# Kernel optimization log

Measured on AMD Instinct MI355X. Metric: run time of the kernel, lower is better.

Reference implementation:

```python
import jax, jax.numpy as jnp
import numpy as np

KERNEL_MUL = 2.0
KERNEL_NUM = 5
EPS = 1e-3


def setup_inputs() -> dict:
    key = jax.random.key(0)
    k1, k2 = jax.random.split(key)
    source = jax.random.normal(k1, (2048, 512), dtype=jnp.float32)
    target = jax.random.normal(k2, (2048, 512), dtype=jnp.float32)
    beta = jnp.ones((KERNEL_NUM,), dtype=jnp.float32) / KERNEL_NUM
    return {"source": source, "target": target, "beta": beta}


def _sq_dists(total):
    # squared Euclidean pairwise distances, (N, N), clamped >= 0 (matches cdist(p=2)**2)
    sq = jnp.sum(total * total, axis=-1)
    d = sq[:, None] + sq[None, :] - 2.0 * (total @ total.T)
    return jnp.maximum(d, 0.0)


def _project_simplex(v):
    m = v.shape[0]
    mu = -jnp.sort(-v)                      # descending
    cs = jnp.cumsum(mu)
    ar = jnp.arange(1, m + 1, dtype=v.dtype)
    cond = mu - (cs - 1.0) / ar > 0
    idx = jnp.where(cond, jnp.arange(m), -1)
    rho = jnp.where(jnp.any(cond), jnp.max(idx), 0)
    theta = (cs[rho] - 1.0) / (rho + 1).astype(v.dtype)
    p = jnp.maximum(v - theta, 0.0)
    return p / (p.sum() + 1e-12)


def _update_beta(source, target, beta):
    # Batched version of the per-pair quad-kernel loop in _update_beta.
    Ns, D = source.shape
    Nt = target.shape[0]
    P = min(Ns // 2, Nt // 2)  # num_effective_pairs (static)
    s = source[: 2 * P].reshape(P, 2, D)
    t = target[: 2 * P].reshape(P, 2, D)
    quad = jnp.concatenate([s, t], axis=1)              # (P, 4, D) -> [s1, s2, t1, t2]
    diff = quad[:, :, None, :] - quad[:, None, :, :]
    sq = jnp.sum(diff * diff, axis=-1)                  # (P, 4, 4)
    offdiag = ~np.eye(4, dtype=bool)
    bw = jnp.median(sq[:, offdiag], axis=1) + 1e-6      # per-pair median of nonzero dists
    bw = bw / (KERNEL_MUL ** (KERNEL_NUM // 2))
    bws = bw[:, None] * (KERNEL_MUL ** jnp.arange(KERNEL_NUM, dtype=bw.dtype))[None, :]
    K = jnp.exp(-sq[:, None, :, :] / bws[:, :, None, None])   # (P, 5, 4, 4)
    g = K[:, :, 0, 1] + K[:, :, 2, 3] - K[:, :, 0, 2] - K[:, :, 1, 3]  # (P, 5)
    gm = jnp.mean(g, axis=0)
    Q = (g.T @ g) / P - jnp.outer(gm, gm) + EPS * jnp.eye(KERNEL_NUM, dtype=g.dtype)
    # projected gradient descent on the simplex (lr=1, max_iter=100, tol=1e-6)
    def cond_fn(st):
        _, _, i, conv = st
        return (i < 100) & (~conv)
    def body_fn(st):
        b, _, i, _ = st
        proj = _project_simplex(b - Q @ b)
        conv = jnp.linalg.norm(proj - b) < 1e-6
        return (proj, proj, i + 1, conv)
    _, proj, _, _ = jax.lax.while_loop(
        cond_fn, body_fn, (beta, beta, jnp.int32(0), jnp.array(False)))
    return proj


def _forward(source, target, beta):
    beta_new = _update_beta(jax.lax.stop_gradient(source),
                            jax.lax.stop_gradient(target), beta)
    Ns = source.shape[0]
    total = jnp.concatenate([source, target], axis=0)   # (N, D)
    N = total.shape[0]
    sq = _sq_dists(total)                               # (N, N)
    offdiag = ~np.eye(N, dtype=bool)
    bw = jnp.median(sq[offdiag]) + 1e-6
    bw = bw / (KERNEL_MUL ** (KERNEL_NUM // 2))
    bws = bw * (KERNEL_MUL ** jnp.arange(KERNEL_NUM, dtype=sq.dtype))  # (5,)
    Ks = jnp.exp(-sq[None, :, :] / bws[:, None, None])  # (5, N, N)
    joint = jnp.einsum('k,kij->ij', beta_new, Ks)
    XX = joint[:Ns, :Ns]
    YY = joint[Ns:, Ns:]
    XY = joint[:Ns, Ns:]
    n = XX.shape[0]
    m = YY.shape[0]
    term_XX = (jnp.sum(XX) - jnp.trace(XX)) / (n * (n - 1))
    term_YY = (jnp.sum(YY) - jnp.trace(YY)) / (m * (m - 1))
    term_XY = jnp.sum(XY) / (n * m)
    loss = term_XX + term_YY - 2.0 * term_XY
    return jnp.maximum(loss, 0.0)


def reference(source, target, beta):
    return _forward(source, target, beta)
```

## Files before the change

### kernel.cpp

```cpp
#include <hip/hip_runtime.h>
#include <math.h>

#define NT 4096
#define NS 2048
#define DDIM 512
#define KN 5
#define NTILES 528

typedef __bf16 bf16x8 __attribute__((ext_vector_type(8)));
typedef float f32x4 __attribute__((ext_vector_type(4)));
typedef unsigned short u16x8 __attribute__((ext_vector_type(8)));

static __device__ inline unsigned short f2bf(float x) {
    unsigned u = __float_as_uint(x);
    unsigned r = (u + 0x7fffu + ((u >> 16) & 1u)) >> 16;
    return (unsigned short)r;
}
static __device__ inline float bf2f(unsigned short h) {
    return __uint_as_float(((unsigned)h) << 16);
}

static __device__ inline void tri_map(int b, int& bx, int& by) {
    int x = (int)((sqrtf(8.0f * (float)b + 1.0f) - 1.0f) * 0.5f);
    while ((x + 1) * (x + 2) / 2 <= b) ++x;
// ... 61 lines not shown
#define CMPSW(x, y) { float hi_ = fmaxf(x, y); float lo_ = fminf(x, y); x = hi_; y = lo_; }
        CMPSW(mu0, mu1) CMPSW(mu3, mu4) CMPSW(mu2, mu4) CMPSW(mu2, mu3)
        CMPSW(mu0, mu3) CMPSW(mu0, mu2) CMPSW(mu1, mu4) CMPSW(mu1, mu3) CMPSW(mu1, mu2)
#undef CMPSW
        float cs0 = mu0, cs1 = cs0 + mu1, cs2 = cs1 + mu2, cs3 = cs2 + mu3, cs4 = cs3 + mu4;
        bool c1 = mu1 * 2.0f > cs1 - 1.0f;
        bool c2 = mu2 * 3.0f > cs2 - 1.0f;
        bool c3 = mu3 * 4.0f > cs3 - 1.0f;
        bool c4 = mu4 * 5.0f > cs4 - 1.0f;
        float csSel = cs0, rcpSel = 1.0f;
        if (c1) { csSel = cs1; rcpSel = 0.5f; }
        if (c2) { csSel = cs2; rcpSel = (1.0f / 3.0f); }
        if (c3) { csSel = cs3; rcpSel = 0.25f; }
        if (c4) { csSel = cs4; rcpSel = 0.2f; }
        float theta = (csSel - 1.0f) * rcpSel;
        float ssum = 0.0f;
        #pragma unroll
        for (int k = 0; k < KN; ++k) { proj[k] = fmaxf(v[k] - theta, 0.0f); ssum += proj[k]; }
        float invs = 1.0f / (ssum + 1e-12f);
        float nd = 0.0f;
        #pragma unroll
        for (int k = 0; k < KN; ++k) {
            proj[k] *= invs;
            float dd = proj[k] - b[k];
            nd += dd * dd;
            b[k] = proj[k];
        }
        if (nd < 1e-12f) break;
    }
    #pragma unroll
    for (int k = 0; k < KN; ++k) beta_out[k] = proj[k];
}

__global__ __launch_bounds__(256) void k_prep2(const float* __restrict__ S,
                                               const float* __restrict__ T,
                                               unsigned short* __restrict__ Hi,
                                               unsigned short* __restrict__ Lo,
                                               float* __restrict__ norms,
                                               float* __restrict__ g,
                                               unsigned* __restrict__ hists,
                                               unsigned* __restrict__ sel)
{
    if (blockIdx.x < 44) hists[blockIdx.x * 256 + threadIdx.x] = 0;
    if (blockIdx.x == 50 && threadIdx.x == 0) {
        sel[0] = 0u; sel[1] = 8386559u;
        sel[2] = 0u; sel[3] = 8386560u;
    }
    int p = blockIdx.x * 4 + (threadIdx.x >> 6);
    int l = threadIdx.x & 63;
    const float* r0 = S + (size_t)(2 * p) * DDIM;
    const float* r1 = r0 + DDIM;
    const float* r2 = T + (size_t)(2 * p) * DDIM;
    const float* r3 = r2 + DDIM;
    float a[8], b[8], c[8], d[8];
    *(float4*)&a[0] = *(const float4*)(r0 + l * 8); *(float4*)&a[4] = *(const float4*)(r0 + l * 8 + 4);
    *(float4*)&b[0] = *(const float4*)(r1 + l * 8); *(float4*)&b[4] = *(const float4*)(r1 + l * 8 + 4);
    *(float4*)&c[0] = *(const float4*)(r2 + l * 8); *(float4*)&c[4] = *(const float4*)(r2 + l * 8 + 4);
    *(float4*)&d[0] = *(const float4*)(r3 + l * 8); *(float4*)&d[4] = *(const float4*)(r3 + l * 8 + 4);

    float n0 = 0, n1 = 0, n2 = 0, n3 = 0;
    float s01 = 0, s23 = 0, s02 = 0, s13 = 0, s03 = 0, s12 = 0;
    u16x8 h0, l0, h1, l1, h2, l2, h3, l3;
    #pragma unroll
    for (int k = 0; k < 8; ++k) {
        float va = a[k], vb = b[k], vc = c[k], vd = d[k];
        n0 += va * va; n1 += vb * vb; n2 += vc * vc; n3 += vd * vd;
        float t01 = va - vb, t23 = vc - vd, t02 = va - vc, t13 = vb - vd;
        s01 += t01*t01; s23 += t23*t23; s02 += t02*t02; s13 += t13*t13;
        float t03 = va - vd, t12 = vb - vc;
        s03 += t03*t03; s12 += t12*t12;
        unsigned short hh;
        hh = f2bf(va); h0[k] = hh; l0[k] = f2bf(va - bf2f(hh));
        hh = f2bf(vb); h1[k] = hh; l1[k] = f2bf(vb - bf2f(hh));
        hh = f2bf(vc); h2[k] = hh; l2[k] = f2bf(vc - bf2f(hh));
        hh = f2bf(vd); h3[k] = hh; l3[k] = f2bf(vd - bf2f(hh));
    }
// ... 5 lines not shown
    *(u16x8*)&Hi[g1] = h1; *(u16x8*)&Lo[g1] = l1;
    *(u16x8*)&Hi[g2] = h2; *(u16x8*)&Lo[g2] = l2;
    *(u16x8*)&Hi[g3] = h3; *(u16x8*)&Lo[g3] = l3;

    #pragma unroll
    for (int m = 32; m > 0; m >>= 1) {
        n0 += __shfl_xor(n0, m); n1 += __shfl_xor(n1, m);
        n2 += __shfl_xor(n2, m); n3 += __shfl_xor(n3, m);
        s01 += __shfl_xor(s01, m); s23 += __shfl_xor(s23, m);
        s02 += __shfl_xor(s02, m); s13 += __shfl_xor(s13, m);
        s03 += __shfl_xor(s03, m); s12 += __shfl_xor(s12, m);
    }
    if (l == 0) {
        norms[2 * p] = n0; norms[2 * p + 1] = n1;
        norms[NS + 2 * p] = n2; norms[NS + 2 * p + 1] = n3;
        float v[6] = { s01, s02, s03, s12, s13, s23 };
        for (int i = 0; i < 5; ++i)
            for (int j = 0; j < 5 - i; ++j)
                if (v[j] > v[j + 1]) { float t = v[j]; v[j] = v[j + 1]; v[j + 1] = t; }
        float med = 0.5f * (v[2] + v[3]);
        float bw = (med + 1e-6f) * 0.25f;
        #pragma unroll
        for (int k = 0; k < KN; ++k) {
            float inv = 1.0f / (bw * (float)(1 << k));
            g[(size_t)p * KN + k] = expf(-s01 * inv) + expf(-s23 * inv)
                                  - expf(-s02 * inv) - expf(-s13 * inv);
        }
    }
}

__global__ __launch_bounds__(256) void k_dist_mfma(const unsigned short* __restrict__ Hi,
                                                   const unsigned short* __restrict__ Lo,
                                                   const float* __restrict__ norms,
                                                   float* __restrict__ D,
                                                   const float* __restrict__ g,
                                                   const float* __restrict__ beta_in,
                                                   float* __restrict__ beta_out)
{
    __shared__ __align__(16) unsigned short sA[2][2][128][32];
    __shared__ __align__(16) unsigned short sB[2][2][128][32];

    if (blockIdx.x == 0) {
        if (threadIdx.x < 64) beta_solve(g, beta_in, beta_out);
        return;
    }

    int bb = blockIdx.x - 1;
    int swz = (bb & 7) * 66 + (bb >> 3);
    int bx, by;
    tri_map(swz, bx, by);
    const int m0 = by * 128, n0 = bx * 128;

    const int tid = threadIdx.x;
    const int w = tid >> 6, l = tid & 63;
    const int wr = w >> 1, wc = w & 1;

    const int chunk = (l & 3) ^ ((((l >> 2) & 3) + ((l >> 4) & 3)) & 3);
    const size_t gA0 = (size_t)(m0 + w * 16 + (l >> 2)) * DDIM + chunk * 8;
    const size_t gA1 = gA0 + (size_t)64 * DDIM;
    const size_t gB0 = (size_t)(n0 + w * 16 + (l >> 2)) * DDIM + chunk * 8;
    const size_t gB1 = gB0 + (size_t)64 * DDIM;
    const unsigned w1024 = w * 1024;

#define GLD(dst, srcptr, goff)                                                      \
    __builtin_amdgcn_global_load_lds(                                               \
        (const __attribute__((address_space(1))) unsigned*)((srcptr) + (goff)),     \
        (__attribute__((address_space(3))) unsigned*)((char*)(dst) + w1024), 16, 0, 0)
#define STAGE(buf, kk)                                  \
    do {                                                \
        GLD(&sA[buf][0][0][0],  Hi, gA0 + (kk));        \
        GLD(&sA[buf][0][64][0], Hi, gA1 + (kk));        \
        GLD(&sA[buf][1][0][0],  Lo, gA0 + (kk));        \
        GLD(&sA[buf][1][64][0], Lo, gA1 + (kk));        \
        GLD(&sB[buf][0][0][0],  Hi, gB0 + (kk));        \
        GLD(&sB[buf][0][64][0], Hi, gB1 + (kk));        \
        GLD(&sB[buf][1][0][0],  Lo, gB0 + (kk));        \
        GLD(&sB[buf][1][64][0], Lo, gB1 + (kk));        \
    } while (0)

    f32x4 acc[4][4] = {};
    const int q = l >> 4;
    const int fr = ((l & 3) + ((l >> 2) & 3)) & 3;
    const unsigned soff = ((unsigned)(q ^ fr)) << 4;
    const unsigned rowbA = (wr * 64 + (l & 15)) * 64 + soff;
    const unsigned rowbB = (wc * 64 + (l & 15)) * 64 + soff;

    STAGE(0, 0);
    __syncthreads();

    #pragma unroll 2
    for (int t = 0; t < 16; ++t) {
        const int cur = t & 1;
        if (t < 15) STAGE(cur ^ 1, (t + 1) * 32);

        bf16x8 ah[4], al[4], bh[4], bl[4];
        #pragma unroll
        for (int m = 0; m < 4; ++m) {
            ah[m] = *(const bf16x8*)((const char*)&sA[cur][0][0][0] + rowbA + m * 1024);
            al[m] = *(const bf16x8*)((const char*)&sA[cur][1][0][0] + rowbA + m * 1024);
        }
        #pragma unroll
        for (int n = 0; n < 4; ++n) {
            bh[n] = *(const bf16x8*)((const char*)&sB[cur][0][0][0] + rowbB + n * 1024);
            bl[n] = *(const bf16x8*)((const char*)&sB[cur][1][0][0] + rowbB + n * 1024);
        }
        #pragma unroll
        for (int m = 0; m < 4; ++m)
            #pragma unroll
            for (int n = 0; n < 4; ++n) {
                acc[m][n] = __builtin_amdgcn_mfma_f32_16x16x32_bf16(bh[n], ah[m], acc[m][n], 0, 0, 0);
                acc[m][n] = __builtin_amdgcn_mfma_f32_16x16x32_bf16(bl[n], ah[m], acc[m][n], 0, 0, 0);
                acc[m][n] = __builtin_amdgcn_mfma_f32_16x16x32_bf16(bh[n], al[m], acc[m][n], 0, 0, 0);
            }
        __syncthreads();
    }
#undef STAGE
#undef GLD

    float* rowbuf = (float*)&sA[0][0][0][0] + w * 1024;
    const int rr = l & 15;
    #pragma unroll
    for (int m = 0; m < 4; ++m) {
        float nrm = norms[m0 + wr * 64 + m * 16 + rr];
        #pragma unroll
        for (int n = 0; n < 4; ++n) {
            int cb = n0 + wc * 64 + n * 16 + (q << 2);
            float4 ncv = *(const float4*)&norms[cb];
            f32x4 a = acc[m][n];
            float4 o;
            o.x = fmaxf(nrm + ncv.x - 2.0f * a[0], 0.0f);
            o.y = fmaxf(nrm + ncv.y - 2.0f * a[1], 0.0f);
            o.z = fmaxf(nrm + ncv.z - 2.0f * a[2], 0.0f);
            o.w = fmaxf(nrm + ncv.w - 2.0f * a[3], 0.0f);
            int ch = (n * 4 + q) ^ (rr & 7);
            *(float4*)(rowbuf + rr * 64 + ch * 4) = o;
        }
        #pragma unroll
        for (int s = 0; s < 4; ++s) {
            int row = s * 4 + q;
            int ch = (l & 15) ^ (row & 7);
            float4 v = *(const float4*)(rowbuf + row * 64 + ch * 4);
            *(float4*)&D[(size_t)(m0 + wr * 64 + m * 16 + row) * NT + n0 + wc * 64 + (l & 15) * 4] = v;
        }
    }
}

__global__ __launch_bounds__(256) void k_hist0_tri(const float* __restrict__ D,
                                                   unsigned* __restrict__ gH)
{
    __shared__ unsigned h[1024];
    for (int i = threadIdx.x; i < 1024; i += 256) h[i] = 0;
    int bx, by;
    tri_map(blockIdx.x, bx, by);
    int m0 = by * 128, n0 = bx * 128;
    unsigned wt = (bx != by) ? 2u : 1u;
    __syncthreads();
    for (int v = threadIdx.x; v < 4096; v += 256) {
        int r = m0 + (v >> 5);
        int c0 = n0 + (v & 31) * 4;
        float4 dv = *(const float4*)&D[(size_t)r * NT + c0];
        const float* dd = (const float*)&dv;
        unsigned pb = __float_as_uint(dd[0]) >> 22;
        unsigned pc = (r == c0) ? 0u : wt;
        #pragma unroll
        for (int j = 1; j < 4; ++j) {
            unsigned bj = __float_as_uint(dd[j]) >> 22;
            unsigned cj = (r == c0 + j) ? 0u : wt;
            if (bj == pb) pc += cj;
            else {
                if (pc) atomicAdd(&h[pb], pc);
                pb = bj; pc = cj;
            }
        }
        if (pc) atomicAdd(&h[pb], pc);
    }
    __syncthreads();
    for (int i = threadIdx.x; i < 1024; i += 256) {
        unsigned c = h[i];
        if (c) atomicAdd(&gH[i], c);
    }
}

__global__ __launch_bounds__(64) void k_scan0(const unsigned* __restrict__ hL0,
                                              unsigned* __restrict__ sel)
{
    int lane = threadIdx.x;
    for (int t = 0; t < 2; ++t) {
        unsigned r = sel[t * 2 + 1];
        unsigned s = 0;
        for (int i = 0; i < 16; ++i) s += hL0[lane * 16 + i];
        unsigned x = s;
        #pragma unroll
        for (int off = 1; off < 64; off <<= 1) {
            unsigned y = __shfl_up(x, off);
            if (lane >= off) x += y;
        }
        unsigned base = x - s;
        bool has = (r >= base) && (r < base + s);
        unsigned long long mm = __ballot(has);
        int leader = __ffsll(mm) - 1;
        unsigned bin = 0, cb = 0;
        if (lane == leader) {
            unsigned cc = base;
            for (int i = 0; i < 16; ++i) {
                unsigned hv = hL0[lane * 16 + i];
                if (r < cc + hv) { bin = lane * 16 + i; cb = cc; break; }
                cc += hv;
            }
        }
        bin = __shfl(bin, leader);
        cb = __shfl(cb, leader);
        if (lane == 0) {
            sel[t * 2 + 0] = bin;
            sel[t * 2 + 1] = r - cb;
        }
    }
}

template<int LEVEL>
__global__ __launch_bounds__(256) void k_hist_tri(const float* __restrict__ D,
                                                  const unsigned* __restrict__ sel,
                                                  unsigned* __restrict__ gA,
                                                  unsigned* __restrict__ gB)
{
    constexpr int NB = (LEVEL == 2) ? 4096 : 1024;
    __shared__ unsigned lha[NB];
    __shared__ unsigned lhb[NB];
    for (int i = threadIdx.x; i < NB; i += 256) { lha[i] = 0; lhb[i] = 0; }
    unsigned pA = sel[0], pB = sel[2];
    int bx, by;
    tri_map(blockIdx.x, bx, by);
    int m0 = by * 128, n0 = bx * 128;
    unsigned wt = (bx != by) ? 2u : 1u;
    __syncthreads();
    for (int v = threadIdx.x; v < 4096; v += 256) {
        int r = m0 + (v >> 5);
        int c0 = n0 + (v & 31) * 4;
        float4 dv = *(const float4*)&D[(size_t)r * NT + c0];
        const float* dd = (const float*)&dv;
        #pragma unroll
        for (int j = 0; j < 4; ++j) {
            if (r == c0 + j) continue;
            unsigned key = __float_as_uint(dd[j]);
            if constexpr (LEVEL == 1) {
                if ((key >> 22) == pA) atomicAdd(&lha[(key >> 12) & 1023], wt);
                if ((key >> 22) == pB) atomicAdd(&lhb[(key >> 12) & 1023], wt);
            } else {
                if ((key >> 12) == pA) atomicAdd(&lha[key & 4095], wt);
                if ((key >> 12) == pB) atomicAdd(&lhb[key & 4095], wt);
            }
        }
    }
    __syncthreads();
    for (int i = threadIdx.x; i < NB; i += 256) {
        unsigned ca = lha[i];
        if (ca) atomicAdd(&gA[i], ca);
        unsigned cb = lhb[i];
        if (cb) atomicAdd(&gB[i], cb);
    }
}

template<int LEVEL>
__global__ __launch_bounds__(64) void k_scan(const unsigned* __restrict__ hA,
                                             const unsigned* __restrict__ hB,
                                             unsigned* __restrict__ sel,
                                             float* __restrict__ params)
{
    constexpr int NB = (LEVEL == 2) ? 4096 : 1024;
    constexpr int C = NB / 64;
    int lane = threadIdx.x;
    for (int t = 0; t < 2; ++t) {
        const unsigned* h = (t == 0 ? hA : hB);
        unsigned r = sel[t * 2 + 1];
        unsigned s = 0;
        for (int i = 0; i < C; ++i) s += h[lane * C + i];
        unsigned x = s;
        #pragma unroll
        for (int off = 1; off < 64; off <<= 1) {
            unsigned y = __shfl_up(x, off);
            if (lane >= off) x += y;
        }
        unsigned base = x - s;
        bool has = (r >= base) && (r < base + s);
        unsigned long long mm = __ballot(has);
        int leader = __ffsll(mm) - 1;
        unsigned bin = 0, cb = 0;
        if (lane == leader) {
            unsigned cc = base;
            for (int i = 0; i < C; ++i) {
                unsigned hv = h[lane * C + i];
                if (r < cc + hv) { bin = lane * C + i; cb = cc; break; }
                cc += hv;
            }
        }
        bin = __shfl(bin, leader);
        cb = __shfl(cb, leader);
        if (lane == 0) {
            if (LEVEL == 1) sel[t * 2 + 0] = (sel[t * 2 + 0] << 10) | bin;
            else            sel[4 + t]     = (sel[t * 2 + 0] << 12) | bin;
            sel[t * 2 + 1] = r - cb;
        }
    }
    if (LEVEL == 2 && lane == 0) {
        float vA = __uint_as_float(sel[4]);
        float vB = __uint_as_float(sel[5]);
        float med = 0.5f * (vA + vB);
        float bw = (med + 1e-6f) * 0.25f;
        #pragma unroll
        for (int k = 0; k < KN; ++k) params[k] = 1.0f / (bw * (float)(1 << k));
    }
}

__global__ __launch_bounds__(256) void k_wsum_tri(const float* __restrict__ D,
                                                  const float* __restrict__ params,
                                                  const float* __restrict__ beta,
                                                  double* __restrict__ partials)
{
    float i0 = params[0], i1 = params[1], i2 = params[2], i3 = params[3], i4 = params[4];
    float b0 = beta[0], b1 = beta[1], b2 = beta[2], b3 = beta[3], b4 = beta[4];
    const double wDiag = 1.0 / ((double)NS * (NS - 1));
    const double wOff = -1.0 / ((double)NS * NS);
    int bx, by;
    tri_map(blockIdx.x, bx, by);
    int m0 = by * 128, n0 = bx * 128;
    double wt = (bx != by) ? 2.0 : 1.0;
    double acc = 0.0;
    for (int v = threadIdx.x; v < 4096; v += 256) {
        int r = m0 + (v >> 5);
        int c0 = n0 + (v & 31) * 4;
        float4 dv = *(const float4*)&D[(size_t)r * NT + c0];
        const float* dd = (const float*)&dv;
        #pragma unroll
        for (int j = 0; j < 4; ++j) {
            int c = c0 + j;
            if (r == c) continue;
            float sq = dd[j];
            float val = b0 * __expf(-sq * i0) + b1 * __expf(-sq * i1) + b2 * __expf(-sq * i2)
                      + b3 * __expf(-sq * i3) + b4 * __expf(-sq * i4);
            bool same = (r < NS) == (c < NS);
            acc += (same ? wDiag : wOff) * (double)val;
        }
    }
    acc *= wt;
    __shared__ double red[256];
    red[threadIdx.x] = acc;
    __syncthreads();
    for (int off = 128; off > 0; off >>= 1) {
        if (threadIdx.x < off) red[threadIdx.x] += red[threadIdx.x + off];
        __syncthreads();
    }
    if (threadIdx.x == 0) partials[blockIdx.x] = red[0];
}

__global__ __launch_bounds__(256) void k_final(const double* __restrict__ partials,
                                               float* __restrict__ out, int count)
{
    double acc = 0;
    for (int i = threadIdx.x; i < count; i += 256) acc += partials[i];
    __shared__ double red[256];
    red[threadIdx.x] = acc;
    __syncthreads();
    for (int off = 128; off > 0; off >>= 1) {
        if (threadIdx.x < off) red[threadIdx.x] += red[threadIdx.x + off];
        __syncthreads();
    }
    if (threadIdx.x == 0) out[0] = (float)fmax(red[0], 0.0);
}

extern "C" void kernel_launch(void* const* d_in, const int* in_sizes, int n_in,
                              void* d_out, int out_size, void* d_ws, size_t ws_size,
                              hipStream_t stream)
{
    const float* S = (const float*)d_in[0];
    const float* T = (const float*)d_in[1];
    const float* beta = (const float*)d_in[2];
    float* out = (float*)d_out;

    float* D = (float*)d_ws;
    unsigned short* Hi = (unsigned short*)(D + (size_t)NT * NT);
    unsigned short* Lo = Hi + (size_t)NT * DDIM;
    float* norms = (float*)(Lo + (size_t)NT * DDIM);
    float* g = norms + NT;
    float* beta2 = g + 1024 * KN;
    float* params = beta2 + 8;
    unsigned* sel = (unsigned*)(params + 8);
    unsigned* hists = sel + 16;
    unsigned* hL0 = hists;
    unsigned* hL1A = hL0 + 1024;
    unsigned* hL1B = hL1A + 1024;
    unsigned* hL2A = hL1B + 1024;
    unsigned* hL2B = hL2A + 4096;
    double* partials = (double*)(hists + 11264);

    k_prep2<<<dim3(256), dim3(256), 0, stream>>>(S, T, Hi, Lo, norms, g, hists, sel);
    k_dist_mfma<<<dim3(NTILES + 1), dim3(256), 0, stream>>>(Hi, Lo, norms, D, g, beta, beta2);
    k_hist0_tri<<<dim3(NTILES), dim3(256), 0, stream>>>(D, hL0);
    k_scan0<<<dim3(1), dim3(64), 0, stream>>>(hL0, sel);
    k_hist_tri<1><<<dim3(NTILES), dim3(256), 0, stream>>>(D, sel, hL1A, hL1B);
    k_scan<1><<<dim3(1), dim3(64), 0, stream>>>(hL1A, hL1B, sel, params);
    k_hist_tri<2><<<dim3(NTILES), dim3(256), 0, stream>>>(D, sel, hL2A, hL2B);
    k_scan<2><<<dim3(1), dim3(64), 0, stream>>>(hL2A, hL2B, sel, params);
    k_wsum_tri<<<dim3(NTILES), dim3(256), 0, stream>>>(D, params, beta2, partials);
    k_final<<<dim3(1), dim3(256), 0, stream>>>(partials, out, NTILES);
}
```

Baseline: 151.7 us.

## Fold scan kernels into histogram tails and triple-buffer GEMM staging

The separate single-block scan and final-reduce kernels are removed. The last block of each histogram or weighted-sum kernel, found with an atomic ticket counter, now does the scan or final reduction itself, which cuts ten launches to six. The distance GEMM moves from double to triple-buffered LDS staging with explicit vmcnt waits and a single barrier per k-step, and the beta solve moves into the first histogram kernel. This removes launch gaps and per-iteration sync stalls, at the cost of more LDS per block (lower occupancy) and reliance on threadfence/atomic ordering.

```diff
diff --git a/kernel.cpp b/kernel.cpp
--- a/kernel.cpp
+++ b/kernel.cpp
@@ -117,6 +117,35 @@
     for (int k = 0; k < KN; ++k) beta_out[k] = proj[k];
 }
 
+static __device__ void scan_find(unsigned* __restrict__ h, int C, unsigned r,
+                                 unsigned& bin, unsigned& rem)
+{
+    int lane = threadIdx.x;
+    unsigned s = 0;
+    for (int i = 0; i < C; ++i) s += atomicAdd(&h[lane * C + i], 0u);
+    unsigned x = s;
+    #pragma unroll
+    for (int off = 1; off < 64; off <<= 1) {
+        unsigned y = __shfl_up(x, off);
+        if (lane >= off) x += y;
+    }
+    unsigned base = x - s;
+    bool has = (r >= base) && (r < base + s);
+    unsigned long long mm = __ballot(has);
+    int leader = __ffsll(mm) - 1;
+    unsigned b = 0, cb = 0;
+    if (lane == leader) {
+        unsigned cc = base;
+        for (int i = 0; i < C; ++i) {
+            unsigned hv = atomicAdd(&h[lane * C + i], 0u);
+            if (r < cc + hv) { b = lane * C + i; cb = cc; break; }
+            cc += hv;
+        }
+    }
+    bin = __shfl(b, leader);
+    rem = r - __shfl(cb, leader);
+}
+
 __global__ __launch_bounds__(256) void k_prep2(const float* __restrict__ S,
                                                const float* __restrict__ T,
                                                unsigned short* __restrict__ Hi,
@@ -126,7 +155,7 @@
                                                unsigned* __restrict__ hists,
                                                unsigned* __restrict__ sel)
 {
-    if (blockIdx.x < 44) hists[blockIdx.x * 256 + threadIdx.x] = 0;
+    if (blockIdx.x < 45) hists[blockIdx.x * 256 + threadIdx.x] = 0;
     if (blockIdx.x == 50 && threadIdx.x == 0) {
         sel[0] = 0u; sel[1] = 8386559u;
         sel[2] = 0u; sel[3] = 8386560u;
@@ -198,20 +227,12 @@
 __global__ __launch_bounds__(256) void k_dist_mfma(const unsigned short* __restrict__ Hi,
                                                    const unsigned short* __restrict__ Lo,
                                                    const float* __restrict__ norms,
-                                                   float* __restrict__ D,
-                                                   const float* __restrict__ g,
-                                                   const float* __restrict__ beta_in,
-                                                   float* __restrict__ beta_out)
-{
-    __shared__ __align__(16) unsigned short sA[2][2][128][32];
-    __shared__ __align__(16) unsigned short sB[2][2][128][32];
-
-    if (blockIdx.x == 0) {
-        if (threadIdx.x < 64) beta_solve(g, beta_in, beta_out);
-        return;
-    }
-
-    int bb = blockIdx.x - 1;
+                                                   float* __restrict__ D)
+{
+    __shared__ __align__(16) unsigned short sA[3][2][128][32];
+    __shared__ __align__(16) unsigned short sB[3][2][128][32];
+
+    int bb = blockIdx.x;
     int swz = (bb & 7) * 66 + (bb >> 3);
     int bx, by;
     tri_map(swz, bx, by);
@@ -252,12 +273,16 @@
     const unsigned rowbB = (wc * 64 + (l & 15)) * 64 + soff;
 
     STAGE(0, 0);
-    __syncthreads();
-
-    #pragma unroll 2
+    STAGE(1, 32);
+
+    #pragma unroll 16
     for (int t = 0; t < 16; ++t) {
-        const int cur = t & 1;
-        if (t < 15) STAGE(cur ^ 1, (t + 1) * 32);
+        const int cur = t % 3;
+        if (t == 15) { asm volatile("s_waitcnt vmcnt(0)" ::: "memory"); }
+        else         { asm volatile("s_waitcnt vmcnt(8)" ::: "memory"); }
+        __builtin_amdgcn_s_barrier();
+        __builtin_amdgcn_sched_barrier(0);
+        if (t < 14) STAGE((t + 2) % 3, (t + 2) * 32);
 
         bf16x8 ah[4], al[4], bh[4], bl[4];
         #pragma unroll
@@ -278,10 +303,10 @@
                 acc[m][n] = __builtin_amdgcn_mfma_f32_16x16x32_bf16(bl[n], ah[m], acc[m][n], 0, 0, 0);
                 acc[m][n] = __builtin_amdgcn_mfma_f32_16x16x32_bf16(bh[n], al[m], acc[m][n], 0, 0, 0);
             }
-        __syncthreads();
     }
 #undef STAGE
 #undef GLD
+    __syncthreads();
 
     float* rowbuf = (float*)&sA[0][0][0][0] + w * 1024;
     const int rr = l & 15;
@@ -311,13 +336,23 @@
     }
 }
 
-__global__ __launch_bounds__(256) void k_hist0_tri(const float* __restrict__ D,
-                                                   unsigned* __restrict__ gH)
-{
+__global__ __launch_bounds__(256) void k_h0s(const float* __restrict__ D,
+                                             const float* __restrict__ g,
+                                             const float* __restrict__ beta_in,
+                                             float* __restrict__ beta_out,
+                                             unsigned* __restrict__ gH,
+                                             unsigned* __restrict__ sel,
+                                             unsigned* __restrict__ cnt)
+{
+    if (blockIdx.x == 0) {
+        if (threadIdx.x < 64) beta_solve(g, beta_in, beta_out);
+        return;
+    }
     __shared__ unsigned h[1024];
+    __shared__ unsigned tk;
     for (int i = threadIdx.x; i < 1024; i += 256) h[i] = 0;
     int bx, by;
-    tri_map(blockIdx.x, bx, by);
+    tri_map(blockIdx.x - 1, bx, by);
     int m0 = by * 128, n0 = bx * 128;
     unsigned wt = (bx != by) ? 2u : 1u;
     __syncthreads();
@@ -345,54 +380,31 @@
         unsigned c = h[i];
         if (c) atomicAdd(&gH[i], c);
     }
-}
-
-__global__ __launch_bounds__(64) void k_scan0(const unsigned* __restrict__ hL0,
-                                              unsigned* __restrict__ sel)
-{
-    int lane = threadIdx.x;
-    for (int t = 0; t < 2; ++t) {
-        unsigned r = sel[t * 2 + 1];
-        unsigned s = 0;
-        for (int i = 0; i < 16; ++i) s += hL0[lane * 16 + i];
-        unsigned x = s;
-        #pragma unroll
-        for (int off = 1; off < 64; off <<= 1) {
-            unsigned y = __shfl_up(x, off);
-            if (lane >= off) x += y;
-        }
-        unsigned base = x - s;
-        bool has = (r >= base) && (r < base + s);
-        unsigned long long mm = __ballot(has);
-        int leader = __ffsll(mm) - 1;
-        unsigned bin = 0, cb = 0;
-        if (lane == leader) {
-            unsigned cc = base;
-            for (int i = 0; i < 16; ++i) {
-                unsigned hv = hL0[lane * 16 + i];
-                if (r < cc + hv) { bin = lane * 16 + i; cb = cc; break; }
-                cc += hv;
+    __syncthreads();
+    if (threadIdx.x == 0) { __threadfence(); tk = atomicAdd(&cnt[0], 1u); }
+    __syncthreads();
+    if (tk == NTILES - 1) {
+        __threadfence();
+        if (threadIdx.x < 64) {
+            for (int t = 0; t < 2; ++t) {
+                unsigned bin, rem;
+                scan_find(gH, 16, sel[t * 2 + 1], bin, rem);
+                if (threadIdx.x == 0) { sel[t * 2 + 0] = bin; sel[t * 2 + 1] = rem; }
             }
         }
-        bin = __shfl(bin, leader);
-        cb = __shfl(cb, leader);
-        if (lane == 0) {
-            sel[t * 2 + 0] = bin;
-            sel[t * 2 + 1] = r - cb;
-        }
-    }
-}
-
-template<int LEVEL>
-__global__ __launch_bounds__(256) void k_hist_tri(const float* __restrict__ D,
-                                                  const unsigned* __restrict__ sel,
-                                                  unsigned* __restrict__ gA,
-                                                  unsigned* __restrict__ gB)
-{
-    constexpr int NB = (LEVEL == 2) ? 4096 : 1024;
-    __shared__ unsigned lha[NB];
-    __shared__ unsigned lhb[NB];
-    for (int i = threadIdx.x; i < NB; i += 256) { lha[i] = 0; lhb[i] = 0; }
+    }
+}
+
+__global__ __launch_bounds__(256) void k_h1s(const float* __restrict__ D,
+                                             unsigned* __restrict__ sel,
+                                             unsigned* __restrict__ gA,
+                                             unsigned* __restrict__ gB,
+                                             unsigned* __restrict__ cnt)
+{
+    __shared__ unsigned lha[1024];
+    __shared__ unsigned lhb[1024];
+    __shared__ unsigned tk;
+    for (int i = threadIdx.x; i < 1024; i += 256) { lha[i] = 0; lhb[i] = 0; }
     unsigned pA = sel[0], pB = sel[2];
     int bx, by;
     tri_map(blockIdx.x, bx, by);
@@ -408,80 +420,104 @@
         for (int j = 0; j < 4; ++j) {
             if (r == c0 + j) continue;
             unsigned key = __float_as_uint(dd[j]);
-            if constexpr (LEVEL == 1) {
-                if ((key >> 22) == pA) atomicAdd(&lha[(key >> 12) & 1023], wt);
-                if ((key >> 22) == pB) atomicAdd(&lhb[(key >> 12) & 1023], wt);
-            } else {
-                if ((key >> 12) == pA) atomicAdd(&lha[key & 4095], wt);
-                if ((key >> 12) == pB) atomicAdd(&lhb[key & 4095], wt);
-            }
-        }
-    }
-    __syncthreads();
-    for (int i = threadIdx.x; i < NB; i += 256) {
+            if ((key >> 22) == pA) atomicAdd(&lha[(key >> 12) & 1023], wt);
+            if ((key >> 22) == pB) atomicAdd(&lhb[(key >> 12) & 1023], wt);
+        }
+    }
+    __syncthreads();
+    for (int i = threadIdx.x; i < 1024; i += 256) {
         unsigned ca = lha[i];
         if (ca) atomicAdd(&gA[i], ca);
         unsigned cb = lhb[i];
         if (cb) atomicAdd(&gB[i], cb);
     }
-}
-
-template<int LEVEL>
-__global__ __launch_bounds__(64) void k_scan(const unsigned* __restrict__ hA,
-                                             const unsigned* __restrict__ hB,
+    __syncthreads();
+    if (threadIdx.x == 0) { __threadfence(); tk = atomicAdd(&cnt[1], 1u); }
+    __syncthreads();
+    if (tk == NTILES - 1) {
+        __threadfence();
+        if (threadIdx.x < 64) {
+            for (int t = 0; t < 2; ++t) {
+                unsigned bin, rem;
+                scan_find(t == 0 ? gA : gB, 16, sel[t * 2 + 1], bin, rem);
+                if (threadIdx.x == 0) {
+                    sel[t * 2 + 0] = (sel[t * 2 + 0] << 10) | bin;
+                    sel[t * 2 + 1] = rem;
+                }
+            }
+        }
+    }
+}
+
+__global__ __launch_bounds__(256) void k_h2s(const float* __restrict__ D,
                                              unsigned* __restrict__ sel,
-                                             float* __restrict__ params)
-{
-    constexpr int NB = (LEVEL == 2) ? 4096 : 1024;
-    constexpr int C = NB / 64;
-    int lane = threadIdx.x;
-    for (int t = 0; t < 2; ++t) {
-        const unsigned* h = (t == 0 ? hA : hB);
-        unsigned r = sel[t * 2 + 1];
-        unsigned s = 0;
-        for (int i = 0; i < C; ++i) s += h[lane * C + i];
-        unsigned x = s;
-        #pragma unroll
-        for (int off = 1; off < 64; off <<= 1) {
-            unsigned y = __shfl_up(x, off);
-            if (lane >= off) x += y;
-        }
-        unsigned base = x - s;
-        bool has = (r >= base) && (r < base + s);
-        unsigned long long mm = __ballot(has);
-        int leader = __ffsll(mm) - 1;
-        unsigned bin = 0, cb = 0;
-        if (lane == leader) {
-            unsigned cc = base;
-            for (int i = 0; i < C; ++i) {
-                unsigned hv = h[lane * C + i];
-                if (r < cc + hv) { bin = lane * C + i; cb = cc; break; }
-                cc += hv;
+                                             unsigned* __restrict__ gA,
+                                             unsigned* __restrict__ gB,
+                                             float* __restrict__ params,
+                                             unsigned* __restrict__ cnt)
+{
+    __shared__ unsigned lha[4096];
+    __shared__ unsigned lhb[4096];
+    __shared__ unsigned tk;
+    for (int i = threadIdx.x; i < 4096; i += 256) { lha[i] = 0; lhb[i] = 0; }
+    unsigned pA = sel[0], pB = sel[2];
+    int bx, by;
+    tri_map(blockIdx.x, bx, by);
+    int m0 = by * 128, n0 = bx * 128;
+    unsigned wt = (bx != by) ? 2u : 1u;
+    __syncthreads();
+    for (int v = threadIdx.x; v < 4096; v += 256) {
+        int r = m0 + (v >> 5);
+        int c0 = n0 + (v & 31) * 4;
+        float4 dv = *(const float4*)&D[(size_t)r * NT + c0];
+        const float* dd = (const float*)&dv;
+        #pragma unroll
+        for (int j = 0; j < 4; ++j) {
+            if (r == c0 + j) continue;
+            unsigned key = __float_as_uint(dd[j]);
+            if ((key >> 12) == pA) atomicAdd(&lha[key & 4095], wt);
+            if ((key >> 12) == pB) atomicAdd(&lhb[key & 4095], wt);
+        }
+    }
+    __syncthreads();
+    for (int i = threadIdx.x; i < 4096; i += 256) {
+        unsigned ca = lha[i];
+        if (ca) atomicAdd(&gA[i], ca);
+        unsigned cb = lhb[i];
+        if (cb) atomicAdd(&gB[i], cb);
+    }
+    __syncthreads();
+    if (threadIdx.x == 0) { __threadfence(); tk = atomicAdd(&cnt[2], 1u); }
+    __syncthreads();
+    if (tk == NTILES - 1) {
+        __threadfence();
+        if (threadIdx.x < 64) {
+            unsigned keyA = 0, keyB = 0;
+            for (int t = 0; t < 2; ++t) {
+                unsigned bin, rem;
+                scan_find(t == 0 ? gA : gB, 64, sel[t * 2 + 1], bin, rem);
+                unsigned key = (sel[t * 2 + 0] << 12) | bin;
+                if (t == 0) keyA = key; else keyB = key;
             }
-        }
-        bin = __shfl(bin, leader);
-        cb = __shfl(cb, leader);
-        if (lane == 0) {
-            if (LEVEL == 1) sel[t * 2 + 0] = (sel[t * 2 + 0] << 10) | bin;
-            else            sel[4 + t]     = (sel[t * 2 + 0] << 12) | bin;
-            sel[t * 2 + 1] = r - cb;
-        }
-    }
-    if (LEVEL == 2 && lane == 0) {
-        float vA = __uint_as_float(sel[4]);
-        float vB = __uint_as_float(sel[5]);
-        float med = 0.5f * (vA + vB);
-        float bw = (med + 1e-6f) * 0.25f;
-        #pragma unroll
-        for (int k = 0; k < KN; ++k) params[k] = 1.0f / (bw * (float)(1 << k));
-    }
-}
-
-__global__ __launch_bounds__(256) void k_wsum_tri(const float* __restrict__ D,
-                                                  const float* __restrict__ params,
-                                                  const float* __restrict__ beta,
-                                                  double* __restrict__ partials)
-{
+            if (threadIdx.x == 0) {
+                float med = 0.5f * (__uint_as_float(keyA) + __uint_as_float(keyB));
+                float bw = (med + 1e-6f) * 0.25f;
+                #pragma unroll
+                for (int k = 0; k < KN; ++k) params[k] = 1.0f / (bw * (float)(1 << k));
+            }
+        }
+    }
+}
+
+__global__ __launch_bounds__(256) void k_wsumf(const float* __restrict__ D,
+                                               const float* __restrict__ params,
+                                               const float* __restrict__ beta,
+                                               double* __restrict__ partials,
+                                               unsigned* __restrict__ cnt,
+                                               float* __restrict__ out)
+{
+    __shared__ double red[256];
+    __shared__ unsigned tk;
     float i0 = params[0], i1 = params[1], i2 = params[2], i3 = params[3], i4 = params[4];
     float b0 = beta[0], b1 = beta[1], b2 = beta[2], b3 = beta[3], b4 = beta[4];
     const double wDiag = 1.0 / ((double)NS * (NS - 1));
@@ -508,29 +544,33 @@
         }
     }
     acc *= wt;
-    __shared__ double red[256];
     red[threadIdx.x] = acc;
     __syncthreads();
     for (int off = 128; off > 0; off >>= 1) {
         if (threadIdx.x < off) red[threadIdx.x] += red[threadIdx.x + off];
         __syncthreads();
     }
-    if (threadIdx.x == 0) partials[blockIdx.x] = red[0];
-}
-
-__global__ __launch_bounds__(256) void k_final(const double* __restrict__ partials,
-                                               float* __restrict__ out, int count)
-{
-    double acc = 0;
-    for (int i = threadIdx.x; i < count; i += 256) acc += partials[i];
-    __shared__ double red[256];
-    red[threadIdx.x] = acc;
-    __syncthreads();
-    for (int off = 128; off > 0; off >>= 1) {
-        if (threadIdx.x < off) red[threadIdx.x] += red[threadIdx.x + off];
+    if (threadIdx.x == 0) {
+        partials[blockIdx.x] = red[0];
+        __threadfence();
+        tk = atomicAdd(&cnt[3], 1u);
+    }
+    __syncthreads();
+    if (tk == NTILES - 1) {
+        __threadfence();
+        double a2 = 0.0;
+        for (int i = threadIdx.x; i < NTILES; i += 256) {
+            unsigned long long u = atomicAdd((unsigned long long*)&partials[i], 0ull);
+            a2 += __longlong_as_double(u);
+        }
+        red[threadIdx.x] = a2;
         __syncthreads();
-    }
-    if (threadIdx.x == 0) out[0] = (float)fmax(red[0], 0.0);
+        for (int off = 128; off > 0; off >>= 1) {
+            if (threadIdx.x < off) red[threadIdx.x] += red[threadIdx.x + off];
+            __syncthreads();
+        }
+        if (threadIdx.x == 0) out[0] = (float)fmax(red[0], 0.0);
+    }
 }
 
 extern "C" void kernel_launch(void* const* d_in, const int* in_sizes, int n_in,
@@ -552,20 +592,17 @@
     unsigned* sel = (unsigned*)(params + 8);
     unsigned* hists = sel + 16;
     unsigned* hL0 = hists;
-    unsigned* hL1A = hL0 + 1024;
-    unsigned* hL1B = hL1A + 1024;
-    unsigned* hL2A = hL1B + 1024;
-    unsigned* hL2B = hL2A + 4096;
-    double* partials = (double*)(hists + 11264);
+    unsigned* hL1A = hists + 1024;
+    unsigned* hL1B = hists + 2048;
+    unsigned* hL2A = hists + 3072;
+    unsigned* hL2B = hists + 7168;
+    unsigned* cnt  = hists + 11264;
+    double* partials = (double*)(hists + 11520);
 
     k_prep2<<<dim3(256), dim3(256), 0, stream>>>(S, T, Hi, Lo, norms, g, hists, sel);
-    k_dist_mfma<<<dim3(NTILES + 1), dim3(256), 0, stream>>>(Hi, Lo, norms, D, g, beta, beta2);
-    k_hist0_tri<<<dim3(NTILES), dim3(256), 0, stream>>>(D, hL0);
-    k_scan0<<<dim3(1), dim3(64), 0, stream>>>(hL0, sel);
-    k_hist_tri<1><<<dim3(NTILES), dim3(256), 0, stream>>>(D, sel, hL1A, hL1B);
-    k_scan<1><<<dim3(1), dim3(64), 0, stream>>>(hL1A, hL1B, sel, params);
-    k_hist_tri<2><<<dim3(NTILES), dim3(256), 0, stream>>>(D, sel, hL2A, hL2B);
-    k_scan<2><<<dim3(1), dim3(64), 0, stream>>>(hL2A, hL2B, sel, params);
-    k_wsum_tri<<<dim3(NTILES), dim3(256), 0, stream>>>(D, params, beta2, partials);
-    k_final<<<dim3(1), dim3(256), 0, stream>>>(partials, out, NTILES);
-}
+    k_dist_mfma<<<dim3(NTILES), dim3(256), 0, stream>>>(Hi, Lo, norms, D);
+    k_h0s<<<dim3(NTILES + 1), dim3(256), 0, stream>>>(D, g, beta, beta2, hL0, sel, cnt);
+    k_h1s<<<dim3(NTILES), dim3(256), 0, stream>>>(D, sel, hL1A, hL1B, cnt);
+    k_h2s<<<dim3(NTILES), dim3(256), 0, stream>>>(D, sel, hL2A, hL2B, params, cnt);
+    k_wsumf<<<dim3(NTILES), dim3(256), 0, stream>>>(D, params, beta2, partials, cnt, out);
+}
```

Result: slower. 202.7 us (+33.7%).

## Restructure median radix select with bf16 key copy and 12/4/16-bit levels

Applied to the files above, without the earlier changes.

The distance kernel now also writes a truncated 16-bit copy of each distance when the workspace is large enough. The first two histogram passes read this half-width copy instead of the fp32 matrix. The radix split changes from 10/10/12 to 12/4/16 bits, with a 65536-bin global-atomic histogram in the last pass and a 256-thread scan kernel. Norms are cached in shared memory in the distance epilogue. This cuts DRAM reads in two of the three selection passes, at the cost of an extra 32MB write, more zeroing work and global atomics in the final pass.

```diff
diff --git a/kernel.cpp b/kernel.cpp
--- a/kernel.cpp
+++ b/kernel.cpp
@@ -117,6 +117,7 @@
     for (int k = 0; k < KN; ++k) beta_out[k] = proj[k];
 }
 
+#define NZERO (4096 + 64 + 64 + 65536 + 65536)
 __global__ __launch_bounds__(256) void k_prep2(const float* __restrict__ S,
                                                const float* __restrict__ T,
                                                unsigned short* __restrict__ Hi,
@@ -126,7 +127,7 @@
                                                unsigned* __restrict__ hists,
                                                unsigned* __restrict__ sel)
 {
-    if (blockIdx.x < 44) hists[blockIdx.x * 256 + threadIdx.x] = 0;
+    for (unsigned i = blockIdx.x * 256 + threadIdx.x; i < NZERO; i += 65536) hists[i] = 0;
     if (blockIdx.x == 50 && threadIdx.x == 0) {
         sel[0] = 0u; sel[1] = 8386559u;
         sel[2] = 0u; sel[3] = 8386560u;
@@ -199,6 +200,8 @@
                                                    const unsigned short* __restrict__ Lo,
                                                    const float* __restrict__ norms,
                                                    float* __restrict__ D,
+                                                   unsigned short* __restrict__ D16,
+                                                   int do16,
                                                    const float* __restrict__ g,
                                                    const float* __restrict__ beta_in,
                                                    float* __restrict__ beta_out)
@@ -283,15 +286,19 @@
 #undef STAGE
 #undef GLD
 
+    float* ncache = (float*)&sB[0][0][0][0];
+    if (tid < 128) ncache[tid] = norms[m0 + tid];
+    else           ncache[tid] = norms[n0 + tid - 128];
+    __syncthreads();
+
     float* rowbuf = (float*)&sA[0][0][0][0] + w * 1024;
     const int rr = l & 15;
     #pragma unroll
     for (int m = 0; m < 4; ++m) {
-        float nrm = norms[m0 + wr * 64 + m * 16 + rr];
+        float nrm = ncache[wr * 64 + m * 16 + rr];
         #pragma unroll
         for (int n = 0; n < 4; ++n) {
-            int cb = n0 + wc * 64 + n * 16 + (q << 2);
-            float4 ncv = *(const float4*)&norms[cb];
+            float4 ncv = *(const float4*)&ncache[128 + wc * 64 + n * 16 + (q << 2)];
             f32x4 a = acc[m][n];
             float4 o;
             o.x = fmaxf(nrm + ncv.x - 2.0f * a[0], 0.0f);
@@ -306,171 +313,259 @@
             int row = s * 4 + q;
             int ch = (l & 15) ^ (row & 7);
             float4 v = *(const float4*)(rowbuf + row * 64 + ch * 4);
-            *(float4*)&D[(size_t)(m0 + wr * 64 + m * 16 + row) * NT + n0 + wc * 64 + (l & 15) * 4] = v;
-        }
-    }
-}
-
-__global__ __launch_bounds__(256) void k_hist0_tri(const float* __restrict__ D,
-                                                   unsigned* __restrict__ gH)
-{
-    __shared__ unsigned h[1024];
-    for (int i = threadIdx.x; i < 1024; i += 256) h[i] = 0;
+            size_t base = (size_t)(m0 + wr * 64 + m * 16 + row) * NT + n0 + wc * 64 + (l & 15) * 4;
+            *(float4*)&D[base] = v;
+            if (do16) {
+                ushort4 u;
+                u.x = (unsigned short)(__float_as_uint(v.x) >> 16);
+                u.y = (unsigned short)(__float_as_uint(v.y) >> 16);
+                u.z = (unsigned short)(__float_as_uint(v.z) >> 16);
+                u.w = (unsigned short)(__float_as_uint(v.w) >> 16);
+                *(ushort4*)&D16[base] = u;
+            }
+        }
+    }
+}
+
+template<bool S16>
+__global__ __launch_bounds__(256) void k_h0(const float* __restrict__ D,
+                                            const unsigned short* __restrict__ D16,
+                                            unsigned* __restrict__ gH)
+{
+    __shared__ unsigned h[4096];
+    for (int i = threadIdx.x; i < 4096; i += 256) h[i] = 0;
     int bx, by;
     tri_map(blockIdx.x, bx, by);
     int m0 = by * 128, n0 = bx * 128;
     unsigned wt = (bx != by) ? 2u : 1u;
     __syncthreads();
+    if constexpr (S16) {
+        for (int v = threadIdx.x; v < 2048; v += 256) {
+            int r = m0 + (v >> 4);
+            int c0 = n0 + (v & 15) * 8;
+            u16x8 dv = *(const u16x8*)&D16[(size_t)r * NT + c0];
+            unsigned pb = (unsigned)dv[0] >> 4;
+            unsigned pc = (r == c0) ? 0u : wt;
+            #pragma unroll
+            for (int j = 1; j < 8; ++j) {
+                unsigned bj = (unsigned)dv[j] >> 4;
+                unsigned cj = (r == c0 + j) ? 0u : wt;
+                if (bj == pb) pc += cj;
+                else { if (pc) atomicAdd(&h[pb], pc); pb = bj; pc = cj; }
+            }
+            if (pc) atomicAdd(&h[pb], pc);
+        }
+    } else {
+        for (int v = threadIdx.x; v < 4096; v += 256) {
+            int r = m0 + (v >> 5);
+            int c0 = n0 + (v & 31) * 4;
+            float4 dv = *(const float4*)&D[(size_t)r * NT + c0];
+            const float* dd = (const float*)&dv;
+            unsigned pb = __float_as_uint(dd[0]) >> 20;
+            unsigned pc = (r == c0) ? 0u : wt;
+            #pragma unroll
+            for (int j = 1; j < 4; ++j) {
+                unsigned bj = __float_as_uint(dd[j]) >> 20;
+                unsigned cj = (r == c0 + j) ? 0u : wt;
+                if (bj == pb) pc += cj;
+                else { if (pc) atomicAdd(&h[pb], pc); pb = bj; pc = cj; }
+            }
+            if (pc) atomicAdd(&h[pb], pc);
+        }
+    }
+    __syncthreads();
+    for (int i = threadIdx.x; i < 4096; i += 256) {
+        unsigned c = h[i];
+        if (c) atomicAdd(&gH[i], c);
+    }
+}
+
+__global__ __launch_bounds__(256) void k_s0(const unsigned* __restrict__ gH,
+                                            unsigned* __restrict__ sel)
+{
+    __shared__ unsigned ls[256];
+    __shared__ unsigned res[4];
+    int tid = threadIdx.x;
+    uint4 a0 = *(const uint4*)&gH[tid * 16 + 0];
+    uint4 a1 = *(const uint4*)&gH[tid * 16 + 4];
+    uint4 a2 = *(const uint4*)&gH[tid * 16 + 8];
+    uint4 a3 = *(const uint4*)&gH[tid * 16 + 12];
+    unsigned V[16] = { a0.x,a0.y,a0.z,a0.w, a1.x,a1.y,a1.z,a1.w,
+                       a2.x,a2.y,a2.z,a2.w, a3.x,a3.y,a3.z,a3.w };
+    unsigned s = 0;
+    #pragma unroll
+    for (int i = 0; i < 16; ++i) s += V[i];
+    ls[tid] = s;
+    __syncthreads();
+    for (int off = 1; off < 256; off <<= 1) {
+        unsigned y = (tid >= off) ? ls[tid - off] : 0u;
+        __syncthreads();
+        ls[tid] += y;
+        __syncthreads();
+    }
+    unsigned incl = ls[tid], base = incl - s;
+    for (int t = 0; t < 2; ++t) {
+        unsigned r = sel[t * 2 + 1];
+        if (r >= base && r < incl) {
+            unsigned cum = base, bin = 0, rem = 0;
+            bool found = false;
+            #pragma unroll
+            for (int i = 0; i < 16; ++i) {
+                unsigned hv = V[i];
+                if (!found && r < cum + hv) { bin = tid * 16 + i; rem = r - cum; found = true; }
+                cum += hv;
+            }
+            res[t * 2] = bin; res[t * 2 + 1] = rem;
+        }
+    }
+    __syncthreads();
+    if (tid == 0) { sel[0] = res[0]; sel[1] = res[1]; sel[2] = res[2]; sel[3] = res[3]; }
+}
+
+template<bool S16>
+__global__ __launch_bounds__(256) void k_h1(const float* __restrict__ D,
+                                            const unsigned short* __restrict__ D16,
+                                            const unsigned* __restrict__ sel,
+                                            unsigned* __restrict__ gA,
+                                            unsigned* __restrict__ gB)
+{
+    __shared__ unsigned ha[16], hb[16];
+    if (threadIdx.x < 16) { ha[threadIdx.x] = 0; hb[threadIdx.x] = 0; }
+    unsigned pA = sel[0], pB = sel[2];
+    int bx, by;
+    tri_map(blockIdx.x, bx, by);
+    int m0 = by * 128, n0 = bx * 128;
+    unsigned wt = (bx != by) ? 2u : 1u;
+    __syncthreads();
+    if constexpr (S16) {
+        for (int v = threadIdx.x; v < 2048; v += 256) {
+            int r = m0 + (v >> 4);
+            int c0 = n0 + (v & 15) * 8;
+            u16x8 dv = *(const u16x8*)&D16[(size_t)r * NT + c0];
+            #pragma unroll
+            for (int j = 0; j < 8; ++j) {
+                if (r == c0 + j) continue;
+                unsigned k16 = dv[j];
+                if ((k16 >> 4) == pA) atomicAdd(&ha[k16 & 15], wt);
+                if ((k16 >> 4) == pB) atomicAdd(&hb[k16 & 15], wt);
+            }
+        }
+    } else {
+        for (int v = threadIdx.x; v < 4096; v += 256) {
+            int r = m0 + (v >> 5);
+            int c0 = n0 + (v & 31) * 4;
+            float4 dv = *(const float4*)&D[(size_t)r * NT + c0];
+            const float* dd = (const float*)&dv;
+            #pragma unroll
+            for (int j = 0; j < 4; ++j) {
+                if (r == c0 + j) continue;
+                unsigned key = __float_as_uint(dd[j]);
+                if ((key >> 20) == pA) atomicAdd(&ha[(key >> 16) & 15], wt);
+                if ((key >> 20) == pB) atomicAdd(&hb[(key >> 16) & 15], wt);
+            }
+        }
+    }
+    __syncthreads();
+    if (threadIdx.x < 16) {
+        unsigned ca = ha[threadIdx.x];
+        if (ca) atomicAdd(&gA[threadIdx.x], ca);
+        unsigned cb = hb[threadIdx.x];
+        if (cb) atomicAdd(&gB[threadIdx.x], cb);
+    }
+}
+
+__global__ __launch_bounds__(64) void k_s1(const unsigned* __restrict__ gA,
+                                           const unsigned* __restrict__ gB,
+                                           unsigned* __restrict__ sel)
+{
+    int lane = threadIdx.x;
+    for (int t = 0; t < 2; ++t) {
+        const unsigned* h = (t == 0) ? gA : gB;
+        unsigned r = sel[t * 2 + 1];
+        unsigned c = (lane < 16) ? h[lane] : 0u;
+        unsigned x = c;
+        #pragma unroll
+        for (int off = 1; off < 16; off <<= 1) {
+            unsigned y = __shfl_up(x, off);
+            if (lane >= off) x += y;
+        }
+        unsigned base = x - c;
+        if (lane < 16 && r >= base && r < base + c) {
+            sel[t * 2 + 0] = (sel[t * 2 + 0] << 4) | (unsigned)lane;
+            sel[t * 2 + 1] = r - base;
+        }
+    }
+}
+
+__global__ __launch_bounds__(256) void k_h2(const float* __restrict__ D,
+                                            const unsigned* __restrict__ sel,
+                                            unsigned* __restrict__ HA,
+                                            unsigned* __restrict__ HB)
+{
+    unsigned pA = sel[0], pB = sel[2];
+    int bx, by;
+    tri_map(blockIdx.x, bx, by);
+    int m0 = by * 128, n0 = bx * 128;
+    unsigned wt = (bx != by) ? 2u : 1u;
     for (int v = threadIdx.x; v < 4096; v += 256) {
         int r = m0 + (v >> 5);
         int c0 = n0 + (v & 31) * 4;
         float4 dv = *(const float4*)&D[(size_t)r * NT + c0];
         const float* dd = (const float*)&dv;
-        unsigned pb = __float_as_uint(dd[0]) >> 22;
-        unsigned pc = (r == c0) ? 0u : wt;
-        #pragma unroll
-        for (int j = 1; j < 4; ++j) {
-            unsigned bj = __float_as_uint(dd[j]) >> 22;
-            unsigned cj = (r == c0 + j) ? 0u : wt;
-            if (bj == pb) pc += cj;
-            else {
-                if (pc) atomicAdd(&h[pb], pc);
-                pb = bj; pc = cj;
-            }
-        }
-        if (pc) atomicAdd(&h[pb], pc);
-    }
-    __syncthreads();
-    for (int i = threadIdx.x; i < 1024; i += 256) {
-        unsigned c = h[i];
-        if (c) atomicAdd(&gH[i], c);
-    }
-}
-
-__global__ __launch_bounds__(64) void k_scan0(const unsigned* __restrict__ hL0,
-                                              unsigned* __restrict__ sel)
-{
-    int lane = threadIdx.x;
-    for (int t = 0; t < 2; ++t) {
-        unsigned r = sel[t * 2 + 1];
-        unsigned s = 0;
-        for (int i = 0; i < 16; ++i) s += hL0[lane * 16 + i];
-        unsigned x = s;
-        #pragma unroll
-        for (int off = 1; off < 64; off <<= 1) {
-            unsigned y = __shfl_up(x, off);
-            if (lane >= off) x += y;
-        }
-        unsigned base = x - s;
-        bool has = (r >= base) && (r < base + s);
-        unsigned long long mm = __ballot(has);
-        int leader = __ffsll(mm) - 1;
-        unsigned bin = 0, cb = 0;
-        if (lane == leader) {
-            unsigned cc = base;
-            for (int i = 0; i < 16; ++i) {
-                unsigned hv = hL0[lane * 16 + i];
-                if (r < cc + hv) { bin = lane * 16 + i; cb = cc; break; }
-                cc += hv;
-            }
-        }
-        bin = __shfl(bin, leader);
-        cb = __shfl(cb, leader);
-        if (lane == 0) {
-            sel[t * 2 + 0] = bin;
-            sel[t * 2 + 1] = r - cb;
-        }
-    }
-}
-
-template<int LEVEL>
-__global__ __launch_bounds__(256) void k_hist_tri(const float* __restrict__ D,
-                                                  const unsigned* __restrict__ sel,
-                                                  unsigned* __restrict__ gA,
-                                                  unsigned* __restrict__ gB)
-{
-    constexpr int NB = (LEVEL == 2) ? 4096 : 1024;
-    __shared__ unsigned lha[NB];
-    __shared__ unsigned lhb[NB];
-    for (int i = threadIdx.x; i < NB; i += 256) { lha[i] = 0; lhb[i] = 0; }
-    unsigned pA = sel[0], pB = sel[2];
-    int bx, by;
-    tri_map(blockIdx.x, bx, by);
-    int m0 = by * 128, n0 = bx * 128;
-    unsigned wt = (bx != by) ? 2u : 1u;
-    __syncthreads();
-    for (int v = threadIdx.x; v < 4096; v += 256) {
-        int r = m0 + (v >> 5);
-        int c0 = n0 + (v & 31) * 4;
-        float4 dv = *(const float4*)&D[(size_t)r * NT + c0];
-        const float* dd = (const float*)&dv;
         #pragma unroll
         for (int j = 0; j < 4; ++j) {
             if (r == c0 + j) continue;
             unsigned key = __float_as_uint(dd[j]);
-            if constexpr (LEVEL == 1) {
-                if ((key >> 22) == pA) atomicAdd(&lha[(key >> 12) & 1023], wt);
-                if ((key >> 22) == pB) atomicAdd(&lhb[(key >> 12) & 1023], wt);
-            } else {
-                if ((key >> 12) == pA) atomicAdd(&lha[key & 4095], wt);
-                if ((key >> 12) == pB) atomicAdd(&lhb[key & 4095], wt);
-            }
-        }
-    }
-    __syncthreads();
-    for (int i = threadIdx.x; i < NB; i += 256) {
-        unsigned ca = lha[i];
-        if (ca) atomicAdd(&gA[i], ca);
-        unsigned cb = lhb[i];
-        if (cb) atomicAdd(&gB[i], cb);
-    }
-}
-
-template<int LEVEL>
-__global__ __launch_bounds__(64) void k_scan(const unsigned* __restrict__ hA,
-                                             const unsigned* __restrict__ hB,
-                                             unsigned* __restrict__ sel,
-                                             float* __restrict__ params)
-{
-    constexpr int NB = (LEVEL == 2) ? 4096 : 1024;
-    constexpr int C = NB / 64;
-    int lane = threadIdx.x;
+            if ((key >> 16) == pA) atomicAdd(&HA[key & 0xffffu], wt);
+            if ((key >> 16) == pB) atomicAdd(&HB[key & 0xffffu], wt);
+        }
+    }
+}
+
+__global__ __launch_bounds__(256) void k_s2(const unsigned* __restrict__ HA,
+                                            const unsigned* __restrict__ HB,
+                                            unsigned* __restrict__ sel,
+                                            float* __restrict__ params)
+{
+    __shared__ unsigned ls[256];
+    __shared__ unsigned keys[2];
+    int tid = threadIdx.x;
     for (int t = 0; t < 2; ++t) {
-        const unsigned* h = (t == 0 ? hA : hB);
+        const unsigned* h = (t == 0) ? HA : HB;
         unsigned r = sel[t * 2 + 1];
         unsigned s = 0;
-        for (int i = 0; i < C; ++i) s += h[lane * C + i];
-        unsigned x = s;
-        #pragma unroll
-        for (int off = 1; off < 64; off <<= 1) {
-            unsigned y = __shfl_up(x, off);
-            if (lane >= off) x += y;
-        }
-        unsigned base = x - s;
-        bool has = (r >= base) && (r < base + s);
-        unsigned long long mm = __ballot(has);
-        int leader = __ffsll(mm) - 1;
-        unsigned bin = 0, cb = 0;
-        if (lane == leader) {
-            unsigned cc = base;
-            for (int i = 0; i < C; ++i) {
-                unsigned hv = h[lane * C + i];
-                if (r < cc + hv) { bin = lane * C + i; cb = cc; break; }
-                cc += hv;
-            }
-        }
-        bin = __shfl(bin, leader);
-        cb = __shfl(cb, leader);
-        if (lane == 0) {
-            if (LEVEL == 1) sel[t * 2 + 0] = (sel[t * 2 + 0] << 10) | bin;
-            else            sel[4 + t]     = (sel[t * 2 + 0] << 12) | bin;
-            sel[t * 2 + 1] = r - cb;
-        }
-    }
-    if (LEVEL == 2 && lane == 0) {
-        float vA = __uint_as_float(sel[4]);
-        float vB = __uint_as_float(sel[5]);
-        float med = 0.5f * (vA + vB);
+        for (int i = 0; i < 64; ++i) {
+            uint4 u = *(const uint4*)&h[tid * 256 + i * 4];
+            s += u.x + u.y + u.z + u.w;
+        }
+        ls[tid] = s;
+        __syncthreads();
+        for (int off = 1; off < 256; off <<= 1) {
+            unsigned y = (tid >= off) ? ls[tid - off] : 0u;
+            __syncthreads();
+            ls[tid] += y;
+            __syncthreads();
+        }
+        unsigned incl = ls[tid], base = incl - s;
+        if (r >= base && r < incl) {
+            unsigned cum = base;
+            unsigned bin = 0;
+            for (int i = 0; i < 64 && cum <= r; ++i) {
+                uint4 u = *(const uint4*)&h[tid * 256 + i * 4];
+                unsigned uu[4] = { u.x, u.y, u.z, u.w };
+                #pragma unroll
+                for (int j = 0; j < 4; ++j) {
+                    if (r < cum + uu[j]) { bin = tid * 256 + i * 4 + j; cum = r + 1; goto done; }
+                    cum += uu[j];
+                }
+            }
+        done:
+            keys[t] = (sel[t * 2] << 16) | bin;
+        }
+        __syncthreads();
+    }
+    if (tid == 0) {
+        float med = 0.5f * (__uint_as_float(keys[0]) + __uint_as_float(keys[1]));
         float bw = (med + 1e-6f) * 0.25f;
         #pragma unroll
         for (int k = 0; k < KN; ++k) params[k] = 1.0f / (bw * (float)(1 << k));
@@ -552,20 +647,33 @@
     unsigned* sel = (unsigned*)(params + 8);
     unsigned* hists = sel + 16;
     unsigned* hL0 = hists;
-    unsigned* hL1A = hL0 + 1024;
-    unsigned* hL1B = hL1A + 1024;
-    unsigned* hL2A = hL1B + 1024;
-    unsigned* hL2B = hL2A + 4096;
-    double* partials = (double*)(hists + 11264);
+    unsigned* h1A = hists + 4096;
+    unsigned* h1B = hists + 4160;
+    unsigned* HA  = hists + 4224;
+    unsigned* HB  = HA + 65536;
+    double* partials = (double*)(HB + 65536);
+    unsigned short* D16 = (unsigned short*)(partials + NTILES);
+
+    size_t need16 = (size_t)((char*)(D16 + (size_t)NT * NT) - (char*)d_ws);
+    int do16 = (ws_size >= need16) ? 1 : 0;
 
     k_prep2<<<dim3(256), dim3(256), 0, stream>>>(S, T, Hi, Lo, norms, g, hists, sel);
-    k_dist_mfma<<<dim3(NTILES + 1), dim3(256), 0, stream>>>(Hi, Lo, norms, D, g, beta, beta2);
-    k_hist0_tri<<<dim3(NTILES), dim3(256), 0, stream>>>(D, hL0);
-    k_scan0<<<dim3(1), dim3(64), 0, stream>>>(hL0, sel);
-    k_hist_tri<1><<<dim3(NTILES), dim3(256), 0, stream>>>(D, sel, hL1A, hL1B);
-    k_scan<1><<<dim3(1), dim3(64), 0, stream>>>(hL1A, hL1B, sel, params);
-    k_hist_tri<2><<<dim3(NTILES), dim3(256), 0, stream>>>(D, sel, hL2A, hL2B);
-    k_scan<2><<<dim3(1), dim3(64), 0, stream>>>(hL2A, hL2B, sel, params);
+    k_dist_mfma<<<dim3(NTILES + 1), dim3(256), 0, stream>>>(Hi, Lo, norms, D, D16, do16,
+                                                            g, beta, beta2);
+    if (do16) {
+        k_h0<true><<<dim3(NTILES), dim3(256), 0, stream>>>(D, D16, hL0);
+    } else {
+        k_h0<false><<<dim3(NTILES), dim3(256), 0, stream>>>(D, D16, hL0);
+    }
+    k_s0<<<dim3(1), dim3(256), 0, stream>>>(hL0, sel);
+    if (do16) {
+        k_h1<true><<<dim3(NTILES), dim3(256), 0, stream>>>(D, D16, sel, h1A, h1B);
+    } else {
+        k_h1<false><<<dim3(NTILES), dim3(256), 0, stream>>>(D, D16, sel, h1A, h1B);
+    }
+    k_s1<<<dim3(1), dim3(64), 0, stream>>>(h1A, h1B, sel);
+    k_h2<<<dim3(NTILES), dim3(256), 0, stream>>>(D, sel, HA, HB);
+    k_s2<<<dim3(1), dim3(256), 0, stream>>>(HA, HB, sel, params);
     k_wsum_tri<<<dim3(NTILES), dim3(256), 0, stream>>>(D, params, beta2, partials);
     k_final<<<dim3(1), dim3(256), 0, stream>>>(partials, out, NTILES);
 }
```

Result: slower. 169.8 us (+12.0%).
